# Kernel optimization log

Measured on AMD Instinct MI355X. Metric: run time of the kernel, lower is better.

## Reference

```python
import jax, jax.numpy as jnp
import numpy as np

C = 256
G = 16
EPS = 1e-5


def conv1x1(x, w):
    # x: [N,C,H,W], w: [Cout,Cin]
    return jnp.einsum('nchw,oc->nohw', x, w)


def group_norm(x, gamma, beta, groups=G, eps=EPS):
    n, c, h, w = x.shape
    xg = x.reshape(n, groups, c // groups, h, w)
    mu = xg.mean(axis=(2, 3, 4), keepdims=True)
    var = ((xg - mu) ** 2).mean(axis=(2, 3, 4), keepdims=True)
    xn = ((xg - mu) * jax.lax.rsqrt(var + eps)).reshape(n, c, h, w)
    return xn * gamma[:, None, None] + beta[:, None, None]


def silu(x):
    return x * jax.nn.sigmoid(x)


def scan(x, axis, reverse=False):
    if reverse:
        return jnp.flip(jnp.cumsum(jnp.flip(x, axis), axis=axis), axis)
    return jnp.cumsum(x, axis=axis)


def depthwise3x3(x, w_dw):
    # w_dw: [C,1,3,3], groups=C
    return jax.lax.conv_general_dilated(
        x, w_dw, window_strides=(1, 1), padding=((1, 1), (1, 1)),
        dimension_numbers=('NCHW', 'OIHW', 'NCHW'), feature_group_count=x.shape[1])


def setup_inputs() -> dict:
    key = jax.random.key(0)
    ks = jax.random.split(key, 5)
    N, H, W = 8, 80, 80
    s1 = 1.0 / np.sqrt(C)
    return {
        'x': jax.random.normal(ks[0], (N, C, H, W), jnp.float32),
        'w_pre': jax.random.normal(ks[1], (C, C), jnp.float32) * s1,
        'g1': jnp.ones((C,), jnp.float32),
        'b1': jnp.zeros((C,), jnp.float32),
        'w_gate': jax.random.normal(ks[2], (C, C), jnp.float32) * s1,
        'b_gate': jnp.zeros((C,), jnp.float32),
        'w_dw': jax.random.normal(ks[3], (C, 1, 3, 3), jnp.float32) * (1.0 / 3.0),
        'w_pw': jax.random.normal(ks[4], (C, C), jnp.float32) * s1,
        'g2': jnp.ones((C,), jnp.float32),
        'b2': jnp.zeros((C,), jnp.float32),
    }


def reference(x, w_pre, g1, b1, w_gate, b_gate, w_dw, w_pw, g2, b2):
    # pre: 1x1 conv -> GroupNorm -> SiLU
    h = silu(group_norm(conv1x1(x, w_pre), g1, b1))
    # 4-directional cumulative scans
    lr = scan(h, 3, False)
    rl = scan(h, 3, True)
    tb = scan(h, 2, False)
    bt = scan(h, 2, True)
    fused = (lr + rl + tb + bt) * 0.25
    # sigmoid gate from pre features
    gate = jax.nn.sigmoid(conv1x1(h, w_gate) + b_gate[:, None, None])
    gated = fused * gate
    # mix: depthwise 3x3 -> 1x1 -> GroupNorm -> SiLU
    y = depthwise3x3(gated, w_dw)
    y = conv1x1(y, w_pw)
    return silu(group_norm(y, g2, b2))
```

## Files before the change

### kernel.cpp

```cpp
#include <hip/hip_runtime.h>
#include <stdint.h>

#define CC 256
#define HH 80
#define WW 80
#define PP 6400
#define GG 16
#define GNCNT (16*6400)
#define SAPAD 272

using frag_ab = __attribute__((ext_vector_type(8))) short;
using frag_cd = __attribute__((ext_vector_type(4))) float;
typedef unsigned short u16;

__device__ __forceinline__ float b2f(u16 u) {
    union { float f; uint32_t i; } v; v.i = ((uint32_t)u) << 16; return v.f;
}
__device__ __forceinline__ u16 f2b(float f) {
    uint32_t x = __float_as_uint(f);
    return (u16)((x + 0x7fffu + ((x >> 16) & 1u)) >> 16);
}
__device__ __forceinline__ float sigf(float x) { return 1.f / (1.f + __expf(-x)); }

__global__ __launch_bounds__(256) void cvt_kernel(const float* __restrict__ src,
                                                  u16* __restrict__ dst, int n4) {
    int i = blockIdx.x * 256 + threadIdx.x;
    if (i < n4) {
        float4 v = ((const float4*)src)[i];
        ushort4 o;
        o.x = f2b(v.x); o.y = f2b(v.y); o.z = f2b(v.z); o.w = f2b(v.w);
        ((ushort4*)dst)[i] = o;
    }
}

template<int MODE>
__global__ __launch_bounds__(256, 3) void gemm_kernel(
    const u16* __restrict__ A,
    const u16* __restrict__ Wb,
    u16* __restrict__ Out,
    float* __restrict__ pstats,
    const float* __restrict__ Srow,
    const float* __restrict__ Scol,
    const float* __restrict__ bgate,
    const float* __restrict__ Xf)
{
    __shared__ __align__(16) u16 sA[64 * SAPAD];

    const int t    = threadIdx.x;
    const int lane = t & 63;
    const int wave = t >> 6;
    const int m    = lane & 15;
    const int q    = lane >> 4;
    const int mt   = blockIdx.x;
    const int m0   = mt * 64;
    const int n    = mt / 100;
    const int o0w  = wave * 64;

    if (MODE == 0) {
        const int cl = t >> 2, pq = t & 3;
        const int p0 = m0 - n * PP;
        #pragma unroll
        for (int cb = 0; cb < 4; cb++) {
            const int c = cb * 64 + cl;
            const float* row = Xf + ((size_t)(n * CC + c)) * PP + p0 + pq * 16;
            #pragma unroll
            for (int u = 0; u < 4; u++) {
                float4 v = ((const float4*)(row + u * 4))[0];
                const int pp = pq * 16 + u * 4;
                sA[(pp + 0) * SAPAD + c] = f2b(v.x);
                sA[(pp + 1) * SAPAD + c] = f2b(v.y);
                sA[(pp + 2) * SAPAD + c] = f2b(v.z);
                sA[(pp + 3) * SAPAD + c] = f2b(v.w);
            }
        }
    } else {
        const int row = t >> 2, qt = t & 3;
        const u16* g = A + (size_t)(m0 + row) * CC + qt * 64;
        u16* d = sA + row * SAPAD + qt * 64;
        #pragma unroll
        for (int i = 0; i < 8; i++)
            *(frag_ab*)(d + i * 8) = *(const frag_ab*)(g + i * 8);
    }
    __syncthreads();

    frag_cd acc[4][4];
    #pragma unroll
    for (int ms = 0; ms < 4; ms++)
        #pragma unroll
        for (int j = 0; j < 4; j++)
            #pragma unroll
            for (int k = 0; k < 4; k++) acc[ms][j][k] = 0.f;

    const u16* wl = Wb + (size_t)(o0w + m) * CC + q * 8;

    #pragma unroll
    for (int jh = 0; jh < 2; jh++) {
        frag_ab wf[2][8];
        #pragma unroll
        for (int jj = 0; jj < 2; jj++)
            #pragma unroll
            for (int kc = 0; kc < 8; kc++)
                wf[jj][kc] = *(const frag_ab*)(wl + (size_t)((jh * 2 + jj) * 16) * CC + kc * 32);
        #pragma unroll
        for (int jj = 0; jj < 2; jj++)
            #pragma unroll
            for (int kc = 0; kc < 8; kc++)
                asm volatile("" : "+v"(wf[jj][kc]));

        #pragma unroll
        for (int ms = 0; ms < 4; ms++) {
            #pragma unroll
            for (int kc = 0; kc < 8; kc++) {
                frag_ab af = *(const frag_ab*)(sA + (ms * 16 + m) * SAPAD + kc * 32 + q * 8);
                #pragma unroll
                for (int jj = 0; jj < 2; jj++)
                    acc[ms][jh * 2 + jj] = __builtin_amdgcn_mfma_f32_16x16x32_bf16(
                        af, wf[jj][kc], acc[ms][jh * 2 + jj], 0, 0, 0);
            }
        }
    }

    ushort4 hv[4][4];
    if (MODE == 1) {
        const int rr0 = lane >> 4;
        const int cH  = o0w + (lane & 15) * 4;
        #pragma unroll
        for (int ms = 0; ms < 4; ms++)
            #pragma unroll
            for (int u = 0; u < 4; u++)
                hv[ms][u] = *(const ushort4*)(sA + (size_t)(ms * 16 + u * 4 + rr0) * SAPAD + cH);
    }
    __syncthreads();

    if (MODE == 0 || MODE == 2) {
        #pragma unroll
        for (int j = 0; j < 4; j++) {
            float s = 0.f, sq = 0.f;
            #pragma unroll
            for (int ms = 0; ms < 4; ms++)
                #pragma unroll
                for (int r = 0; r < 4; r++) {
                    float v = acc[ms][j][r];
                    s += v; sq += v * v;
                }
            #pragma unroll
            for (int off = 32; off > 0; off >>= 1) {
                s  += __shfl_down(s, off);
                sq += __shfl_down(sq, off);
            }
            if (lane == 0) {
                float* p = pstats + (size_t)mt * 32;
                p[wave * 4 + j]      = s;
                p[16 + wave * 4 + j] = sq;
            }
        }
        u16* myT = sA + wave * 1152;
        #pragma unroll
        for (int ms = 0; ms < 4; ms++) {
            #pragma unroll
            for (int j = 0; j < 4; j++)
                #pragma unroll
                for (int r = 0; r < 4; r++)
                    myT[(q * 4 + r) * 72 + j * 16 + m] = f2b(acc[ms][j][r]);
            #pragma unroll
            for (int u = 0; u < 2; u++) {
                const int rr = u * 8 + (lane >> 3);
                frag_ab v = *(const frag_ab*)(myT + rr * 72 + (lane & 7) * 8);
                *(frag_ab*)(Out + (size_t)(m0 + ms * 16 + rr) * CC + o0w + (lane & 7) * 8) = v;
            }
        }
    } else {
        float* myG = (float*)sA + wave * 1152;
        float bg[4];
        #pragma unroll
        for (int j = 0; j < 4; j++) bg[j] = bgate[o0w + j * 16 + m];
        #pragma unroll
        for (int ms = 0; ms < 4; ms++) {
            #pragma unroll
            for (int j = 0; j < 4; j++)
                #pragma unroll
                for (int r = 0; r < 4; r++)
                    myG[(q * 4 + r) * 72 + j * 16 + m] = sigf(acc[ms][j][r] + bg[j]);
            #pragma unroll
            for (int u = 0; u < 4; u++) {
                const int rr  = u * 4 + (lane >> 4);
                const int col = (lane & 15) * 4;
                float4 g4 = *(const float4*)(myG + rr * 72 + col);
                const int row = m0 + ms * 16 + rr;
                const int pl  = row - n * PP;
                const int pr  = pl / WW;
                const int pc  = pl - pr * WW;
                const int o   = o0w + col;
                ushort4 hq = hv[ms][u];
                float4  sr = *(const float4*)(Srow + (size_t)(n * HH + pr) * CC + o);
                float4  sc = *(const float4*)(Scol + (size_t)(n * HH + pc) * CC + o);
                ushort4 ov;
                ov.x = f2b(0.25f * (sr.x + sc.x + 2.f * b2f(hq.x)) * g4.x);
                ov.y = f2b(0.25f * (sr.y + sc.y + 2.f * b2f(hq.y)) * g4.y);
                ov.z = f2b(0.25f * (sr.z + sc.z + 2.f * b2f(hq.z)) * g4.z);
                ov.w = f2b(0.25f * (sr.w + sc.w + 2.f * b2f(hq.w)) * g4.w);
                *(ushort4*)(Out + (size_t)row * CC + o) = ov;
            }
        }
    }
}

__global__ __launch_bounds__(256) void gn1_kernel(
    const u16* __restrict__ c1, u16* __restrict__ hb,
    float* __restrict__ Srow,
    const float* __restrict__ pscr,
    const float* __restrict__ g1, const float* __restrict__ b1)
{
    __shared__ float sred[8 * 256];
    __shared__ float sstat[32];
    const int i = blockIdx.x, n = blockIdx.y;
    const int t = threadIdx.x;
    if (t < 32) {
        const int kind = t >> 4, g = t & 15;
        const float* p = pscr + (size_t)(n * 100) * 32 + kind * 16 + g;
        float s = 0.f;
        #pragma unroll 4
        for (int ii = 0; ii < 100; ii++) s += p[ii * 32];
        sstat[t] = s;
    }
    __syncthreads();

    const int jg = t >> 5, cc = t & 31;
    const int c8 = cc * 8;
    const int g  = cc >> 1;
    const float su   = sstat[g];
    const float sq   = sstat[16 + g];
    const float mean = su * (1.f / GNCNT);
    const float var  = sq * (1.f / GNCNT) - mean * mean;
    const float inv  = rsqrtf(var + 1e-5f);
    float a[8], b[8];
    #pragma unroll
    for (int k = 0; k < 8; k++) {
        a[k] = inv * g1[c8 + k];
        b[k] = b1[c8 + k] - mean * a[k];
    }
    float srow8[8];
    #pragma unroll
    for (int k = 0; k < 8; k++) srow8[k] = 0.f;

    const size_t base = (size_t)(n * PP + i * WW) * CC;
    for (int s = 0; s < 10; s++) {
        const int j = jg + s * 8;
        const u16* src = c1 + base + (size_t)j * CC + c8;
        u16*       dst = hb + base + (size_t)j * CC + c8;
        frag_ab v = *(const frag_ab*)src;
        frag_ab o;
        #pragma unroll
        for (int k = 0; k < 8; k++) {
            float xn = b2f((u16)v[k]) * a[k] + b[k];
            float hs = xn * sigf(xn);
            o[k] = (short)f2b(hs);
            srow8[k] += hs;
        }
        *(frag_ab*)dst = o;
    }
    #pragma unroll
    for (int k = 0; k < 8; k++) sred[jg * 256 + c8 + k] = srow8[k];
    __syncthreads();
    {
        const int c = t;
        float s = 0.f;
        #pragma unroll
        for (int k = 0; k < 8; k++) s += sred[k * 256 + c];
        Srow[(size_t)(n * HH + i) * CC + c] = s;
    }
}

__global__ __launch_bounds__(256) void scol_kernel(
    const u16* __restrict__ hb, float* __restrict__ Scol)
{
    const int jg = blockIdx.x, iq = blockIdx.y, n = blockIdx.z;
    const int t = threadIdx.x;
    const int js = t >> 5, cc = t & 31;
    const int j = jg * 8 + js, c8 = cc * 8;
    float acc8[8];
    #pragma unroll
    for (int k = 0; k < 8; k++) acc8[k] = 0.f;
    for (int s = 0; s < 20; s++) {
        const int i = iq * 20 + s;
        frag_ab v = *(const frag_ab*)(hb + (size_t)(n * PP + i * WW + j) * CC + c8);
        #pragma unroll
        for (int k = 0; k < 8; k++) acc8[k] += b2f((u16)v[k]);
    }
    float* dst = Scol + (size_t)(n * HH + j) * CC + c8;
    #pragma unroll
    for (int k = 0; k < 8; k++) atomicAdd(&dst[k], acc8[k]);
}

__global__ __launch_bounds__(256) void dw_kernel(
    const u16* __restrict__ gin, u16* __restrict__ dout,
    const float* __restrict__ wdw)
{
    __shared__ float sw[1152];
    const int i = blockIdx.x, chalf = blockIdx.y, n = blockIdx.z;
    const int t = threadIdx.x;
    for (int u = t; u < 1152; u += 256) sw[u] = wdw[chalf * 1152 + u];
    __syncthreads();

    const int jg = t >> 5, cc = t & 31;
    const int gc = chalf * 128 + cc * 4;
    float wl[4][9];
    #pragma unroll
    for (int cl = 0; cl < 4; cl++)
        #pragma unroll
        for (int k = 0; k < 9; k++) wl[cl][k] = sw[(cc * 4 + cl) * 9 + k];

    const size_t nbase = (size_t)n * PP * CC;
    for (int s = 0; s < 10; s++) {
        const int j = jg + s * 8;
        float acc4[4] = {0.f, 0.f, 0.f, 0.f};
        #pragma unroll
        for (int di = -1; di <= 1; di++) {
            const int ii = i + di;
            if (ii < 0 || ii >= HH) continue;
            #pragma unroll
            for (int dj = -1; dj <= 1; dj++) {
                const int jj = j + dj;
                if (jj < 0 || jj >= WW) continue;
                ushort4 v = *(const ushort4*)(gin + nbase + (size_t)(ii * WW + jj) * CC + gc);
                const int k = (di + 1) * 3 + (dj + 1);
                acc4[0] += wl[0][k] * b2f(v.x);
                acc4[1] += wl[1][k] * b2f(v.y);
                acc4[2] += wl[2][k] * b2f(v.z);
                acc4[3] += wl[3][k] * b2f(v.w);
            }
        }
        ushort4 o;
        o.x = f2b(acc4[0]); o.y = f2b(acc4[1]); o.z = f2b(acc4[2]); o.w = f2b(acc4[3]);
        *(ushort4*)(dout + nbase + (size_t)(i * WW + j) * CC + gc) = o;
    }
}

__global__ __launch_bounds__(256) void gn2T_kernel(
    const u16* __restrict__ Y, float* __restrict__ out,
    const float* __restrict__ pscr,
    const float* __restrict__ g2, const float* __restrict__ b2v)
{
    __shared__ u16 sT[64 * 72];
    __shared__ float sstat[32];
    const int p0 = blockIdx.x * 64, c0 = blockIdx.y * 64, n = blockIdx.z;
    const int t = threadIdx.x;
    if (t < 32) {
        const int kind = t >> 4, g = t & 15;
        const float* p = pscr + (size_t)(n * 100) * 32 + kind * 16 + g;
        float s = 0.f;
        #pragma unroll 4
        for (int ii = 0; ii < 100; ii++) s += p[ii * 32];
        sstat[t] = s;
    }
    {
        const int pl = t >> 2, cq = t & 3;
        const u16* row = Y + (size_t)(n * PP + p0 + pl) * CC + c0 + cq * 16;
        *(frag_ab*)(sT + pl * 72 + cq * 16)     = *(const frag_ab*)(row);
        *(frag_ab*)(sT + pl * 72 + cq * 16 + 8) = *(const frag_ab*)(row + 8);
    }
    __syncthreads();
    {
        const int cl = t >> 2, pq = t & 3;
        const int c = c0 + cl, g = c >> 4;
        const float su   = sstat[g];
        const float sq   = sstat[16 + g];
        const float mean = su * (1.f / GNCNT);
        const float var  = sq * (1.f / GNCNT) - mean * mean;
        const float inv  = rsqrtf(var + 1e-5f);
        const float a    = inv * g2[c];
        const float b    = b2v[c] - mean * a;
        float* orow = out + (size_t)(n * CC + c) * PP + p0 + pq * 16;
        #pragma unroll
        for (int u4 = 0; u4 < 4; u4++) {
            float4 o;
            float* op = (float*)&o;
            #pragma unroll
            for (int e = 0; e < 4; e++) {
                const int pp = pq * 16 + u4 * 4 + e;
                float xn = b2f(sT[pp * 72 + cl]) * a + b;
                op[e] = xn * sigf(xn);
            }
            ((float4*)(orow + u4 * 4))[0] = o;
        }
    }
}

extern "C" void kernel_launch(void* const* d_in, const int* in_sizes, int n_in,
                              void* d_out, int out_size, void* d_ws, size_t ws_size,
                              hipStream_t stream)
{
    const float* x      = (const float*)d_in[0];
    const float* w_pre  = (const float*)d_in[1];
    const float* g1     = (const float*)d_in[2];
    const float* b1     = (const float*)d_in[3];
    const float* w_gate = (const float*)d_in[4];
    const float* b_gate = (const float*)d_in[5];
    const float* w_dw   = (const float*)d_in[6];
    const float* w_pw   = (const float*)d_in[7];
    const float* g2     = (const float*)d_in[8];
    const float* b2     = (const float*)d_in[9];
    float* out = (float*)d_out;

    char* ws = (char*)d_ws;
    u16*   wb0   = (u16*)(ws);
    u16*   wb1   = (u16*)(ws + 131072);
    u16*   wb2   = (u16*)(ws + 262144);
    u16*   bufA  = (u16*)(ws + 26607616);
    u16*   bufB  = (u16*)(ws + 52822016);
    float* Srow  = (float*)(ws + 79036416);
    float* Scol  = (float*)(ws + 79691776);
    float* pscr0 = (float*)(ws + 80347136);
    float* pscr1 = (float*)(ws + 80449536);

    hipMemsetAsync(Scol, 0, 655360, stream);

    cvt_kernel<<<64, 256, 0, stream>>>(w_pre,  wb0, 16384);
    cvt_kernel<<<64, 256, 0, stream>>>(w_gate, wb1, 16384);
    cvt_kernel<<<64, 256, 0, stream>>>(w_pw,   wb2, 16384);

    gemm_kernel<0><<<800, 256, 0, stream>>>(nullptr, wb0, bufA, pscr0,
                                            nullptr, nullptr, nullptr, x);
    gn1_kernel<<<dim3(80, 8), 256, 0, stream>>>(bufA, bufB, Srow, pscr0, g1, b1);
    scol_kernel<<<dim3(10, 4, 8), 256, 0, stream>>>(bufB, Scol);
    gemm_kernel<1><<<800, 256, 0, stream>>>(bufB, wb1, bufA, nullptr,
                                            Srow, Scol, b_gate, nullptr);
    dw_kernel<<<dim3(80, 2, 8), 256, 0, stream>>>(bufA, bufB, w_dw);
    gemm_kernel<2><<<800, 256, 0, stream>>>(bufB, wb2, bufA, pscr1,
                                            nullptr, nullptr, nullptr, nullptr);
    gn2T_kernel<<<dim3(100, 4, 8), 256, 0, stream>>>(bufA, out, pscr1, g2, b2);
}
```

Measured before the change: 305.6 us.

## Merge weight conversions, replace Scol atomics with partials, widen depthwise kernel

The three weight-conversion launches are merged into one kernel, and the Scol memset plus atomicAdd reduction is replaced by per-quarter partial sums that the gate GEMM epilogue adds up. The depthwise kernel now covers all 256 channels per block with 8-wide bf16 vector loads, using a transposed shared weight layout. This removes two launches and a memset and cuts atomic traffic, at the cost of four extra Scol loads per output element in the GEMM epilogue. The depthwise grid also shrinks by half, which lowers parallelism.

```diff
diff --git a/kernel.cpp b/kernel.cpp
--- a/kernel.cpp
+++ b/kernel.cpp
@@ -22,15 +22,19 @@
 }
 __device__ __forceinline__ float sigf(float x) { return 1.f / (1.f + __expf(-x)); }
 
-__global__ __launch_bounds__(256) void cvt_kernel(const float* __restrict__ src,
-                                                  u16* __restrict__ dst, int n4) {
-    int i = blockIdx.x * 256 + threadIdx.x;
-    if (i < n4) {
-        float4 v = ((const float4*)src)[i];
-        ushort4 o;
-        o.x = f2b(v.x); o.y = f2b(v.y); o.z = f2b(v.z); o.w = f2b(v.w);
-        ((ushort4*)dst)[i] = o;
-    }
+__global__ __launch_bounds__(256) void cvt3_kernel(
+    const float* __restrict__ s0, const float* __restrict__ s1,
+    const float* __restrict__ s2,
+    u16* __restrict__ d0, u16* __restrict__ d1, u16* __restrict__ d2)
+{
+    const int blk = blockIdx.x >> 6;
+    const int i = (blockIdx.x & 63) * 256 + threadIdx.x;
+    const float* s = (blk == 0) ? s0 : (blk == 1) ? s1 : s2;
+    u16*         d = (blk == 0) ? d0 : (blk == 1) ? d1 : d2;
+    float4 v = ((const float4*)s)[i];
+    ushort4 o;
+    o.x = f2b(v.x); o.y = f2b(v.y); o.z = f2b(v.z); o.w = f2b(v.w);
+    ((ushort4*)d)[i] = o;
 }
 
 template<int MODE>
@@ -40,7 +44,7 @@
     u16* __restrict__ Out,
     float* __restrict__ pstats,
     const float* __restrict__ Srow,
-    const float* __restrict__ Scol,
+    const float* __restrict__ Scolp,
     const float* __restrict__ bgate,
     const float* __restrict__ Xf)
 {
@@ -193,7 +197,12 @@
                 const int o   = o0w + col;
                 ushort4 hq = hv[ms][u];
                 float4  sr = *(const float4*)(Srow + (size_t)(n * HH + pr) * CC + o);
-                float4  sc = *(const float4*)(Scol + (size_t)(n * HH + pc) * CC + o);
+                float4 sc; sc.x = sc.y = sc.z = sc.w = 0.f;
+                #pragma unroll
+                for (int iq = 0; iq < 4; iq++) {
+                    float4 v = *(const float4*)(Scolp + ((size_t)((iq * 8 + n) * HH + pc)) * CC + o);
+                    sc.x += v.x; sc.y += v.y; sc.z += v.z; sc.w += v.w;
+                }
                 ushort4 ov;
                 ov.x = f2b(0.25f * (sr.x + sc.x + 2.f * b2f(hq.x)) * g4.x);
                 ov.y = f2b(0.25f * (sr.y + sc.y + 2.f * b2f(hq.y)) * g4.y);
@@ -272,7 +281,7 @@
 }
 
 __global__ __launch_bounds__(256) void scol_kernel(
-    const u16* __restrict__ hb, float* __restrict__ Scol)
+    const u16* __restrict__ hb, float* __restrict__ Scolp)
 {
     const int jg = blockIdx.x, iq = blockIdx.y, n = blockIdx.z;
     const int t = threadIdx.x;
@@ -287,33 +296,38 @@
         #pragma unroll
         for (int k = 0; k < 8; k++) acc8[k] += b2f((u16)v[k]);
     }
-    float* dst = Scol + (size_t)(n * HH + j) * CC + c8;
-    #pragma unroll
-    for (int k = 0; k < 8; k++) atomicAdd(&dst[k], acc8[k]);
+    float* dst = Scolp + ((size_t)((iq * 8 + n) * HH + j)) * CC + c8;
+    *(float4*)(dst)     = make_float4(acc8[0], acc8[1], acc8[2], acc8[3]);
+    *(float4*)(dst + 4) = make_float4(acc8[4], acc8[5], acc8[6], acc8[7]);
 }
 
 __global__ __launch_bounds__(256) void dw_kernel(
     const u16* __restrict__ gin, u16* __restrict__ dout,
     const float* __restrict__ wdw)
 {
-    __shared__ float sw[1152];
-    const int i = blockIdx.x, chalf = blockIdx.y, n = blockIdx.z;
+    __shared__ float sw[2304];
+    const int i = blockIdx.x, n = blockIdx.y;
     const int t = threadIdx.x;
-    for (int u = t; u < 1152; u += 256) sw[u] = wdw[chalf * 1152 + u];
+    for (int u = t; u < 2304; u += 256) {
+        const int c = u / 9, k = u - c * 9;
+        sw[k * 256 + c] = wdw[u];
+    }
     __syncthreads();
 
     const int jg = t >> 5, cc = t & 31;
-    const int gc = chalf * 128 + cc * 4;
-    float wl[4][9];
-    #pragma unroll
-    for (int cl = 0; cl < 4; cl++)
-        #pragma unroll
-        for (int k = 0; k < 9; k++) wl[cl][k] = sw[(cc * 4 + cl) * 9 + k];
+    const int gc = cc * 8;
+    float4 wla[9], wlb[9];
+    #pragma unroll
+    for (int k = 0; k < 9; k++) {
+        wla[k] = *(const float4*)(sw + k * 256 + gc);
+        wlb[k] = *(const float4*)(sw + k * 256 + gc + 4);
+    }
 
     const size_t nbase = (size_t)n * PP * CC;
     for (int s = 0; s < 10; s++) {
         const int j = jg + s * 8;
-        float acc4[4] = {0.f, 0.f, 0.f, 0.f};
+        float a0 = 0.f, a1 = 0.f, a2 = 0.f, a3 = 0.f;
+        float a4 = 0.f, a5 = 0.f, a6 = 0.f, a7 = 0.f;
         #pragma unroll
         for (int di = -1; di <= 1; di++) {
             const int ii = i + di;
@@ -322,17 +336,21 @@
             for (int dj = -1; dj <= 1; dj++) {
                 const int jj = j + dj;
                 if (jj < 0 || jj >= WW) continue;
-                ushort4 v = *(const ushort4*)(gin + nbase + (size_t)(ii * WW + jj) * CC + gc);
+                frag_ab v = *(const frag_ab*)(gin + nbase + (size_t)(ii * WW + jj) * CC + gc);
                 const int k = (di + 1) * 3 + (dj + 1);
-                acc4[0] += wl[0][k] * b2f(v.x);
-                acc4[1] += wl[1][k] * b2f(v.y);
-                acc4[2] += wl[2][k] * b2f(v.z);
-                acc4[3] += wl[3][k] * b2f(v.w);
-            }
-        }
-        ushort4 o;
-        o.x = f2b(acc4[0]); o.y = f2b(acc4[1]); o.z = f2b(acc4[2]); o.w = f2b(acc4[3]);
-        *(ushort4*)(dout + nbase + (size_t)(i * WW + j) * CC + gc) = o;
+                const float4 wa = wla[k], wb = wlb[k];
+                a0 += wa.x * b2f((u16)v[0]); a1 += wa.y * b2f((u16)v[1]);
+                a2 += wa.z * b2f((u16)v[2]); a3 += wa.w * b2f((u16)v[3]);
+                a4 += wb.x * b2f((u16)v[4]); a5 += wb.y * b2f((u16)v[5]);
+                a6 += wb.z * b2f((u16)v[6]); a7 += wb.w * b2f((u16)v[7]);
+            }
+        }
+        frag_ab o;
+        o[0] = (short)f2b(a0); o[1] = (short)f2b(a1);
+        o[2] = (short)f2b(a2); o[3] = (short)f2b(a3);
+        o[4] = (short)f2b(a4); o[5] = (short)f2b(a5);
+        o[6] = (short)f2b(a6); o[7] = (short)f2b(a7);
+        *(frag_ab*)(dout + nbase + (size_t)(i * WW + j) * CC + gc) = o;
     }
 }
 
@@ -406,26 +424,22 @@
     u16*   wb0   = (u16*)(ws);
     u16*   wb1   = (u16*)(ws + 131072);
     u16*   wb2   = (u16*)(ws + 262144);
+    float* Scolp = (float*)(ws + 393216);
     u16*   bufA  = (u16*)(ws + 26607616);
     u16*   bufB  = (u16*)(ws + 52822016);
     float* Srow  = (float*)(ws + 79036416);
-    float* Scol  = (float*)(ws + 79691776);
     float* pscr0 = (float*)(ws + 80347136);
     float* pscr1 = (float*)(ws + 80449536);
 
-    hipMemsetAsync(Scol, 0, 655360, stream);
-
-    cvt_kernel<<<64, 256, 0, stream>>>(w_pre,  wb0, 16384);
-    cvt_kernel<<<64, 256, 0, stream>>>(w_gate, wb1, 16384);
-    cvt_kernel<<<64, 256, 0, stream>>>(w_pw,   wb2, 16384);
+    cvt3_kernel<<<192, 256, 0, stream>>>(w_pre, w_gate, w_pw, wb0, wb1, wb2);
 
     gemm_kernel<0><<<800, 256, 0, stream>>>(nullptr, wb0, bufA, pscr0,
                                             nullptr, nullptr, nullptr, x);
     gn1_kernel<<<dim3(80, 8), 256, 0, stream>>>(bufA, bufB, Srow, pscr0, g1, b1);
-    scol_kernel<<<dim3(10, 4, 8), 256, 0, stream>>>(bufB, Scol);
+    scol_kernel<<<dim3(10, 4, 8), 256, 0, stream>>>(bufB, Scolp);
     gemm_kernel<1><<<800, 256, 0, stream>>>(bufB, wb1, bufA, nullptr,
-                                            Srow, Scol, b_gate, nullptr);
-    dw_kernel<<<dim3(80, 2, 8), 256, 0, stream>>>(bufA, bufB, w_dw);
+                                            Srow, Scolp, b_gate, nullptr);
+    dw_kernel<<<dim3(80, 8), 256, 0, stream>>>(bufA, bufB, w_dw);
     gemm_kernel<2><<<800, 256, 0, stream>>>(bufB, wb2, bufA, pscr1,
                                             nullptr, nullptr, nullptr, nullptr);
     gn2T_kernel<<<dim3(100, 4, 8), 256, 0, stream>>>(bufA, out, pscr1, g2, b2);
```

Measured after the change: 281.7 us. 7.8% less time.
